# Kernel optimization log

Measured on AMD Instinct MI355X. Metric: run time of the kernel, lower is better.

## Reference

```python
import jax, jax.numpy as jnp
import numpy as np

EPS = 1e-8


def setup_inputs() -> dict:
    key = jax.random.key(0)
    num_users, num_items, deg = 8192, 4096, 48
    # Each item j interacts with `deg` DISTINCT users (stride 769 is odd -> coprime
    # with 8192, so offsets are distinct mod num_users). Edges are grouped by item
    # in order, so the original module's max_users_per_item truncation (200 > 48)
    # is inactive and duplicate (user,item) pairs never occur.
    j = np.repeat(np.arange(num_items), deg)
    off = np.tile(np.arange(deg), num_items)
    u = (j * 131 + off * 769) % num_users
    edge_index_ui = jnp.asarray(np.stack([u, j]), dtype=jnp.int32)  # (2, M)
    k1, k2, k3, k4 = jax.random.split(key, 4)
    fraud_u = jax.random.uniform(k1, (num_users,), dtype=jnp.float32)
    fraud_i = jax.random.uniform(k2, (num_items,), dtype=jnp.float32)
    theta = 0.1 * jax.random.normal(k3, (num_items,), dtype=jnp.float32)
    gamma_u = 0.1 * jax.random.normal(k4, (1,), dtype=jnp.float32)
    return {
        "edge_index_ui": edge_index_ui,
        "fraud_u": fraud_u,
        "fraud_i": fraud_i,
        "theta": theta,
        "gamma_u": gamma_u,
        "num_users": num_users,
        "num_items": num_items,
        "topk": 5,
    }


def reference(edge_index_ui, fraud_u, fraud_i, theta, gamma_u, num_users, num_items, topk):
    """Dense-matrix equivalent of LearnableProjector.forward.

    Output is the dense user-user weight matrix W [num_users, num_users]:
    W[s, d] = normalized edge weight of (s -> d) after per-source top-k pruning,
    0 where no edge survives. Equals the original's sparse (edge_index_uu,
    edge_weight) scattered densely (edges are symmetric before per-row top-k).
    """
    u_idx = edge_index_ui[0]
    i_idx = edge_index_ui[1]
    M = u_idx.shape[0]
    ones = jnp.ones((M,), dtype=fraud_u.dtype)

    deg_u = jax.ops.segment_sum(ones, u_idx, num_segments=num_users)
    deg_i = jax.ops.segment_sum(ones, i_idx, num_segments=num_items)

    g_u = gamma_u.reshape(())
    s_u = jnp.log1p(deg_u) * jnp.exp(g_u * fraud_u)   # [U]
    s_i = jnp.log1p(deg_i)                            # [I]; use_item_gamma=False -> fraud_i unused
    w_i = jax.nn.softplus(theta) + EPS                # [I]

    # per-edge value: sqrt(s_u[u]) * sqrt(s_i[i]) * sqrt(w_i[i])
    val_e = jnp.sqrt(s_u + EPS)[u_idx] * jnp.sqrt(s_i + EPS)[i_idx] * jnp.sqrt(w_i)[i_idx]

    # bipartite incidence with values: B[j, u] = val of edge (u, j)
    B = jnp.zeros((num_items, num_users), dtype=val_e.dtype).at[i_idx, u_idx].add(val_e)

    # user-user co-occurrence: P[u, v] = sum_j val(u,j) * val(v,j)
    P = B.T @ B                                        # [U, U]
    diag = jnp.arange(num_users)
    P = P.at[diag, diag].set(0.0)                      # original never forms self-pairs

    # per-source top-k pruning (keep each row's k largest weights)
    kth = jax.lax.top_k(P, topk)[0][:, -1:]            # [U, 1]
    kept = jnp.where(P >= kth, P, 0.0)

    # global max-normalization of surviving edge weights
    return kept / (kept.max() + EPS)
```

## Files before the change

kernel.cpp:

```cpp
#include <hip/hip_runtime.h>
#include <math.h>


#define EPSF 1e-8f
constexpr int U     = 8192;
constexpr int NI    = 4096;
constexpr int DEG   = 48;
constexpr int TOPK  = 5;
constexpr int MAXDU = 48;
constexpr int NTB   = 256;
constexpr int NT    = 128;
constexpr int WPB   = NT / 64;
constexpr int SLOTS = 2048;

typedef float f32x4 __attribute__((ext_vector_type(4)));

#define INS(val, idx)                                                         \
  if ((val) > tv4) {                                                          \
    if ((val) > tv2) {                                                        \
      if ((val) > tv1) {                                                      \
        if ((val) > tv0) { tv4=tv3;ti4=ti3; tv3=tv2;ti3=ti2; tv2=tv1;ti2=ti1; tv1=tv0;ti1=ti0; tv0=(val);ti0=(idx); } \
        else             { tv4=tv3;ti4=ti3; tv3=tv2;ti3=ti2; tv2=tv1;ti2=ti1; tv1=(val);ti1=(idx); }                   \
      } else             { tv4=tv3;ti4=ti3; tv3=tv2;ti3=ti2; tv2=(val);ti2=(idx); } \
    } else {                                                                  \
      if ((val) > tv3)   { tv4=tv3;ti4=ti3; tv3=(val);ti3=(idx); }            \
      else               { tv4=(val);ti4=(idx); }                             \
    }                                                                         \
  }

#define REP36(F) F(0)F(1)F(2)F(3)F(4)F(5)F(6)F(7)F(8)F(9)F(10)F(11)F(12)F(13)\
F(14)F(15)F(16)F(17)F(18)F(19)F(20)F(21)F(22)F(23)F(24)F(25)F(26)F(27)F(28)\
F(29)F(30)F(31)F(32)F(33)F(34)F(35)

#define FILL(r) int pv##r = -1; float pw##r = 0.f;                            \
  { int x = lane + 64 * (r);                                                  \
    if (x < total) {                                                          \
      int k = x / DEG;                      \
      int e = shj[wid][k] + (x - k * DEG);                                    \
      int vv = uidx[e]; pw##r = val_e[e];                                     \
      if (vv != u) pv##r = vv; } }

#define SCAT(r) { int d = pv##r - base;                                       \
  if ((unsigned)d < (unsigned)SLOTS) atomicAdd(&B[d], pw##r); }

#define PASS(P) {                                                             \
  const int base = (P) * SLOTS;                                               \
  _Pragma("unroll") for (int q = 0; q < 8; ++q) Bv[lane + 64 * q] = zz4;      \
  asm volatile("s_waitcnt lgkmcnt(0)" ::: "memory");                          \
  REP36(SCAT)                                                                 \
  asm volatile("s_waitcnt lgkmcnt(0)" ::: "memory");                          \
  _Pragma("unroll") for (int q = 0; q < 8; ++q) {                             \
    f32x4 s4 = Bv[lane + 64 * q];                                             \
    int col0 = base + (lane + 64 * q) * 4;                                    \
    if (s4.x > 0.f) { float vl = au * s4.x; INS(vl, col0)     }               \
    if (s4.y > 0.f) { float vl = au * s4.y; INS(vl, col0 + 1) }               \
    if (s4.z > 0.f) { float vl = au * s4.z; INS(vl, col0 + 2) }               \
    if (s4.w > 0.f) { float vl = au * s4.w; INS(vl, col0 + 3) }               \
  }                                                                           \
  asm volatile("s_waitcnt lgkmcnt(0)" ::: "memory");                          \
  _Pragma("unroll") for (int q = 0; q < 8; ++q)                               \
    __builtin_nontemporal_store(zz4, &orow[(P) * 512 + lane + 64 * q]);       \
}

__global__ __launch_bounds__(NTB) void k_build(
    const int* __restrict__ uidx, const int* __restrict__ iidx, int M,
    int* __restrict__ cnt, int* __restrict__ degi, int* __restrict__ items) {
  int e = blockIdx.x * NTB + threadIdx.x;
  if (e >= M) return;
  int u = uidx[e];
  int j = iidx[e];
  atomicAdd(&degi[j], 1);
  int slot = atomicAdd(&cnt[u], 1);
  if (slot < MAXDU) items[u * MAXDU + slot] = j;
}

__global__ __launch_bounds__(NTB) void k_scalars(
    const int* __restrict__ cnt, const int* __restrict__ degi,
    const float* __restrict__ fraud_u, const float* __restrict__ theta,
    const float* __restrict__ gamma, float* __restrict__ a, float* __restrict__ t) {
  int i = blockIdx.x * NTB + threadIdx.x;
  float g = gamma[0];
  if (i < U) {
    float su = log1pf((float)cnt[i]) * expf(g * fraud_u[i]);
    a[i] = sqrtf(su + EPSF);
  }
  if (i < NI) {
    float w  = log1pf(expf(theta[i])) + EPSF;
    float si = log1pf((float)degi[i]);
    t[i] = (si + EPSF) * w;
  }
}

__global__ __launch_bounds__(NTB) void k_edges(
    const int* __restrict__ uidx, const int* __restrict__ iidx, int M,
    const float* __restrict__ a, const float* __restrict__ t,
    float* __restrict__ val_e) {
  int e = blockIdx.x * NTB + threadIdx.x;
  if (e >= M) return;
  val_e[e] = t[iidx[e]] * a[uidx[e]];
}

__global__ __launch_bounds__(NT, 2) void k_main(
    const int* __restrict__ uidx, const int* __restrict__ cnt,
    const int* __restrict__ items, const float* __restrict__ a,
    const float* __restrict__ val_e, float* __restrict__ val5,
    int* __restrict__ idx5, unsigned* __restrict__ gmax,
    float* __restrict__ out) {
  __shared__ float bkt[WPB][SLOTS];
  __shared__ int   shj[WPB][MAXDU];

  const int tid = threadIdx.x, lane = tid & 63, wid = tid >> 6;
  const int u = blockIdx.x * WPB + wid;
  float* B  = bkt[wid];
  f32x4* Bv = reinterpret_cast<f32x4*>(B);
  f32x4* orow = reinterpret_cast<f32x4*>(out + (size_t)u * U);
  const f32x4 zz4 = {0.f, 0.f, 0.f, 0.f};

  int c = cnt[u]; if (c > MAXDU) c = MAXDU;
  if (lane < c) shj[wid][lane] = items[u * MAXDU + lane] * DEG;
  const int total = c * DEG;
  const float au = a[u];

  REP36(FILL)

  float tv0=-1.f,tv1=-1.f,tv2=-1.f,tv3=-1.f,tv4=-1.f;
  int   ti0=-1,  ti1=-1,  ti2=-1,  ti3=-1,  ti4=-1;

  PASS(0) PASS(1) PASS(2) PASS(3)

#pragma unroll
  for (int it = 0; it < TOPK; ++it) {
    float bv = tv0; int bi = ti0;
    for (int s = 32; s; s >>= 1) {
      float ov = __shfl_xor(bv, s);
      int   oi = __shfl_xor(bi, s);
      if (ov > bv || (ov == bv && oi < bi)) { bv = ov; bi = oi; }
    }
    if (bi >= 0 && ti0 == bi) {
      tv0=tv1;ti0=ti1; tv1=tv2;ti1=ti2; tv2=tv3;ti2=ti3; tv3=tv4;ti3=ti4;
      tv4=-1.f;ti4=-1;
    }
    if (lane == 0) {
      float sv = bv > 0.f ? bv : 0.f;
      val5[u * TOPK + it] = sv;
      idx5[u * TOPK + it] = bi;
      if (it == 0) atomicMax(gmax, __float_as_uint(sv));
    }
  }
}

__global__ __launch_bounds__(NTB) void k_norm(
    const float* __restrict__ val5, const int* __restrict__ idx5,
    const unsigned* __restrict__ gmax, float* __restrict__ out) {
  int i = blockIdx.x * NTB + threadIdx.x;
  if (i >= U * TOPK) return;
  int ix = idx5[i];
  float v = val5[i];
  if (ix >= 0 && v > 0.f) {
    float inv = 1.f / (__uint_as_float(*gmax) + EPSF);
    out[(size_t)(i / TOPK) * U + ix] = v * inv;
  }
}

extern "C" void kernel_launch(void* const* d_in, const int* in_sizes, int n_in,
                              void* d_out, int out_size, void* d_ws, size_t ws_size,
                              hipStream_t stream) {
  const int M = in_sizes[0] / 2;
  const int* uidx = (const int*)d_in[0];
  const int* iidx = uidx + M;
  const float* fraud_u = (const float*)d_in[1];
  const float* theta = (const float*)d_in[3];
  const float* gamma = (const float*)d_in[4];

  int* ws = (int*)d_ws;
  int*      cnt   = ws;
  int*      degi  = ws + U;
  unsigned* gmax  = (unsigned*)(ws + U + NI);
  float*    a     = (float*)(ws + U + NI + 4);
  float*    t     = a + U;
  float*    val5  = t + NI;
  int*      idx5  = (int*)(val5 + U * TOPK);
  int*      items = idx5 + U * TOPK;
  float*    val_e = (float*)(items + U * MAXDU);
  float* out = (float*)d_out;

  (void)hipMemsetAsync(d_ws, 0, (size_t)(U + NI + 4) * sizeof(int), stream);
  k_build  <<<(M + NTB - 1) / NTB, NTB, 0, stream>>>(uidx, iidx, M, cnt, degi, items);
  k_scalars<<<U / NTB,             NTB, 0, stream>>>(cnt, degi, fraud_u, theta, gamma, a, t);
  k_edges  <<<(M + NTB - 1) / NTB, NTB, 0, stream>>>(uidx, iidx, M, a, t, val_e);
  k_main   <<<U / WPB,             NT,  0, stream>>>(uidx, cnt, items, a, val_e,
                                                     val5, idx5, gmax, out);
  k_norm   <<<(U * TOPK + NTB - 1) / NTB, NTB, 0, stream>>>(val5, idx5, gmax, out);
}
```

Baseline: 197.4 us.

## Split zero-fill and co-occurrence work into separate single-wave blocks with full-row LDS

The main kernel now launches two 64-thread blocks per user. Odd blocks only zero-fill the 32 KB output row with nontemporal stores. Even blocks build the entire 8192-wide co-occurrence row in LDS in one pass instead of four 2048-slot passes, then run the top-5 scan. The goal is to overlap the bandwidth-bound output zeroing with the LDS-atomic work and to stop re-reading the edge lists on every pass. The cost is 32 KB of LDS per single-wave block, which limits occupancy, and the zero-fill blocks and compute blocks now finish in an order that is no longer controlled.

```diff
diff --git a/kernel.cpp b/kernel.cpp
--- a/kernel.cpp
+++ b/kernel.cpp
@@ -9,9 +9,7 @@
 constexpr int TOPK  = 5;
 constexpr int MAXDU = 48;
 constexpr int NTB   = 256;
-constexpr int NT    = 128;
-constexpr int WPB   = NT / 64;
-constexpr int SLOTS = 2048;
+constexpr int NCW   = MAXDU * DEG / 64;
 
 typedef float f32x4 __attribute__((ext_vector_type(4)));
 
@@ -27,40 +25,6 @@
       else               { tv4=(val);ti4=(idx); }                             \
     }                                                                         \
   }
-
-#define REP36(F) F(0)F(1)F(2)F(3)F(4)F(5)F(6)F(7)F(8)F(9)F(10)F(11)F(12)F(13)\
-F(14)F(15)F(16)F(17)F(18)F(19)F(20)F(21)F(22)F(23)F(24)F(25)F(26)F(27)F(28)\
-F(29)F(30)F(31)F(32)F(33)F(34)F(35)
-
-#define FILL(r) int pv##r = -1; float pw##r = 0.f;                            \
-  { int x = lane + 64 * (r);                                                  \
-    if (x < total) {                                                          \
-      int k = x / DEG;                      \
-      int e = shj[wid][k] + (x - k * DEG);                                    \
-      int vv = uidx[e]; pw##r = val_e[e];                                     \
-      if (vv != u) pv##r = vv; } }
-
-#define SCAT(r) { int d = pv##r - base;                                       \
-  if ((unsigned)d < (unsigned)SLOTS) atomicAdd(&B[d], pw##r); }
-
-#define PASS(P) {                                                             \
-  const int base = (P) * SLOTS;                                               \
-  _Pragma("unroll") for (int q = 0; q < 8; ++q) Bv[lane + 64 * q] = zz4;      \
-  asm volatile("s_waitcnt lgkmcnt(0)" ::: "memory");                          \
-  REP36(SCAT)                                                                 \
-  asm volatile("s_waitcnt lgkmcnt(0)" ::: "memory");                          \
-  _Pragma("unroll") for (int q = 0; q < 8; ++q) {                             \
-    f32x4 s4 = Bv[lane + 64 * q];                                             \
-    int col0 = base + (lane + 64 * q) * 4;                                    \
-    if (s4.x > 0.f) { float vl = au * s4.x; INS(vl, col0)     }               \
-    if (s4.y > 0.f) { float vl = au * s4.y; INS(vl, col0 + 1) }               \
-    if (s4.z > 0.f) { float vl = au * s4.z; INS(vl, col0 + 2) }               \
-    if (s4.w > 0.f) { float vl = au * s4.w; INS(vl, col0 + 3) }               \
-  }                                                                           \
-  asm volatile("s_waitcnt lgkmcnt(0)" ::: "memory");                          \
-  _Pragma("unroll") for (int q = 0; q < 8; ++q)                               \
-    __builtin_nontemporal_store(zz4, &orow[(P) * 512 + lane + 64 * q]);       \
-}
 
 __global__ __launch_bounds__(NTB) void k_build(
     const int* __restrict__ uidx, const int* __restrict__ iidx, int M,
@@ -100,33 +64,59 @@
   val_e[e] = t[iidx[e]] * a[uidx[e]];
 }
 
-__global__ __launch_bounds__(NT, 2) void k_main(
+__global__ __launch_bounds__(64) void k_main(
     const int* __restrict__ uidx, const int* __restrict__ cnt,
     const int* __restrict__ items, const float* __restrict__ a,
     const float* __restrict__ val_e, float* __restrict__ val5,
     int* __restrict__ idx5, unsigned* __restrict__ gmax,
     float* __restrict__ out) {
-  __shared__ float bkt[WPB][SLOTS];
-  __shared__ int   shj[WPB][MAXDU];
+  __shared__ float Brow[U];
+  __shared__ int   shj[MAXDU];
 
-  const int tid = threadIdx.x, lane = tid & 63, wid = tid >> 6;
-  const int u = blockIdx.x * WPB + wid;
-  float* B  = bkt[wid];
-  f32x4* Bv = reinterpret_cast<f32x4*>(B);
+  const int b = blockIdx.x, lane = threadIdx.x;
+  const int u = b >> 1;
   f32x4* orow = reinterpret_cast<f32x4*>(out + (size_t)u * U);
   const f32x4 zz4 = {0.f, 0.f, 0.f, 0.f};
 
+  if (b & 1) {
+#pragma unroll
+    for (int q = 0; q < U / 4 / 64; ++q)
+      __builtin_nontemporal_store(zz4, &orow[q * 64 + lane]);
+    return;
+  }
+
   int c = cnt[u]; if (c > MAXDU) c = MAXDU;
-  if (lane < c) shj[wid][lane] = items[u * MAXDU + lane] * DEG;
+  if (lane < c) shj[lane] = items[u * MAXDU + lane] * DEG;
+  f32x4* Bv = reinterpret_cast<f32x4*>(Brow);
+#pragma unroll
+  for (int q = 0; q < U / 4 / 64; ++q) Bv[q * 64 + lane] = zz4;
+  asm volatile("s_waitcnt lgkmcnt(0)" ::: "memory");
+
   const int total = c * DEG;
+#pragma unroll
+  for (int r = 0; r < NCW; ++r) {
+    int x = lane + 64 * r;
+    if (x < total) {
+      int k = x / DEG;
+      int e = shj[k] + (x - k * DEG);
+      int v = uidx[e];
+      if (v != u) atomicAdd(&Brow[v], val_e[e]);
+    }
+  }
+  asm volatile("s_waitcnt lgkmcnt(0)" ::: "memory");
+
   const float au = a[u];
-
-  REP36(FILL)
-
   float tv0=-1.f,tv1=-1.f,tv2=-1.f,tv3=-1.f,tv4=-1.f;
   int   ti0=-1,  ti1=-1,  ti2=-1,  ti3=-1,  ti4=-1;
-
-  PASS(0) PASS(1) PASS(2) PASS(3)
+#pragma unroll
+  for (int q = 0; q < U / 4 / 64; ++q) {
+    f32x4 s4 = Bv[q * 64 + lane];
+    int col0 = (q * 64 + lane) * 4;
+    if (s4.x > 0.f) { float vl = au * s4.x; INS(vl, col0)     }
+    if (s4.y > 0.f) { float vl = au * s4.y; INS(vl, col0 + 1) }
+    if (s4.z > 0.f) { float vl = au * s4.z; INS(vl, col0 + 2) }
+    if (s4.w > 0.f) { float vl = au * s4.w; INS(vl, col0 + 3) }
+  }
 
 #pragma unroll
   for (int it = 0; it < TOPK; ++it) {
@@ -188,7 +178,7 @@
   k_build  <<<(M + NTB - 1) / NTB, NTB, 0, stream>>>(uidx, iidx, M, cnt, degi, items);
   k_scalars<<<U / NTB,             NTB, 0, stream>>>(cnt, degi, fraud_u, theta, gamma, a, t);
   k_edges  <<<(M + NTB - 1) / NTB, NTB, 0, stream>>>(uidx, iidx, M, a, t, val_e);
-  k_main   <<<U / WPB,             NT,  0, stream>>>(uidx, cnt, items, a, val_e,
+  k_main   <<<2 * U,               64,  0, stream>>>(uidx, cnt, items, a, val_e,
                                                      val5, idx5, gmax, out);
   k_norm   <<<(U * TOPK + NTB - 1) / NTB, NTB, 0, stream>>>(val5, idx5, gmax, out);
 }
```

Result: slower. 412.4 us (+108.9%).
